# Kernel optimization log

Measured on AMD Instinct MI355X. Metric: run time of the kernel, lower is better.

Reference implementation:

```python
import jax, jax.numpy as jnp
import numpy as np

DIM, H, D = 2048, 16, 128
D_C, D_CQ, D_ROPE = 512, 1536, 64
B, T = 2, 2048


def _rope(t, cos, sin):
    # t: [..., T, D_ROPE]; cos/sin: [T, D_ROPE//2] broadcast over leading dims
    h = D_ROPE // 2
    t1, t2 = t[..., :h], t[..., h:]
    return jnp.concatenate([t1 * cos - t2 * sin, t2 * cos + t1 * sin], axis=-1)


def setup_inputs() -> dict:
    key = jax.random.key(0)
    ks = jax.random.split(key, 10)
    init = lambda k, shp, fan: (jax.random.normal(k, shp, jnp.float32) / np.sqrt(fan).astype(np.float32))
    x = jax.random.normal(ks[0], (B, T, DIM), jnp.float32)
    # RoPE tables for d_rope//2 = 32 rotary channels
    inv_freq = 1.0 / (10000.0 ** (np.arange(0, D_ROPE // 2, dtype=np.float32) / (D_ROPE // 2)))
    ang = np.arange(T, dtype=np.float32)[:, None] * inv_freq[None, :]
    cos = jnp.asarray(np.cos(ang), jnp.float32)
    sin = jnp.asarray(np.sin(ang), jnp.float32)
    return {
        "x": x,
        "cos": cos,
        "sin": sin,
        "w_kv": init(ks[1], (DIM, D_C), DIM),          # kv_compress
        "w_kdec": init(ks[2], (D_C, H * D), D_C),       # k_decompress
        "w_vdec": init(ks[3], (D_C, H * D), D_C),       # v_decompress
        "w_qc": init(ks[4], (DIM, D_CQ), DIM),          # q_compress
        "w_qdec": init(ks[5], (D_CQ, H * D), D_CQ),     # q_decompress
        "w_krope": init(ks[6], (DIM, D_ROPE), DIM),     # k_rope_proj
        "w_qrope": init(ks[7], (DIM, D_ROPE), DIM),     # q_rope_proj
        "w_o": init(ks[8], (H * D, DIM), H * D),        # wo
    }


def reference(x, cos, sin, w_kv, w_kdec, w_vdec, w_qc, w_qdec, w_krope, w_qrope, w_o):
    Bx, Tx, _ = x.shape
    # latent compress -> decompress
    c_kv = x @ w_kv                                       # [B,T,d_c]
    k = (c_kv @ w_kdec).reshape(Bx, Tx, H, D).transpose(0, 2, 1, 3)  # [B,H,T,D]
    v = (c_kv @ w_vdec).reshape(Bx, Tx, H, D).transpose(0, 2, 1, 3)
    c_q = x @ w_qc
    q = (c_q @ w_qdec).reshape(Bx, Tx, H, D).transpose(0, 2, 1, 3)
    # RoPE branch: head-shared projections, rotated then broadcast across heads
    k_rope = _rope(x @ w_krope, cos, sin)                 # [B,T,d_rope]
    q_rope = _rope(x @ w_qrope, cos, sin)
    rope_dim = min(D_ROPE, D)
    qr = jnp.broadcast_to(q_rope[:, None, :, :rope_dim], (Bx, H, Tx, rope_dim))
    kr = jnp.broadcast_to(k_rope[:, None, :, :rope_dim], (Bx, H, Tx, rope_dim))
    q = jnp.concatenate([q[..., :-rope_dim], qr], axis=-1)
    k = jnp.concatenate([k[..., :-rope_dim], kr], axis=-1)
    # causal SDPA, scale = 1/sqrt(head_dim)
    scores = jnp.einsum("bhtd,bhsd->bhts", q, k) / np.float32(np.sqrt(D))
    causal = jnp.tril(jnp.ones((Tx, Tx), dtype=bool))
    scores = jnp.where(causal, scores, jnp.float32(-1e30))
    attn = jax.nn.softmax(scores, axis=-1)
    out = jnp.einsum("bhts,bhsd->bhtd", attn, v)
    out = out.transpose(0, 2, 1, 3).reshape(Bx, Tx, H * D)
    return out @ w_o
```

## Files before the change

### kernel.cpp

```cpp
#include <hip/hip_runtime.h>
#include <stdint.h>
#include <math.h>

#define B_    2
#define T_    2048
#define DIM_  2048
#define H_    16
#define DC_   512
#define DCQ_  1536
#define NROWS (B_*T_)

typedef unsigned short u16;
typedef __attribute__((ext_vector_type(8))) __bf16 bf16x8;
typedef __attribute__((ext_vector_type(4))) float  f32x4;
typedef __attribute__((ext_vector_type(8))) unsigned short u16x8;
typedef __attribute__((ext_vector_type(4))) float  f4v;

__device__ __forceinline__ u16 f2bf(float f){
  unsigned u = __float_as_uint(f);
  u += 0x7FFFu + ((u >> 16) & 1u);
  return (u16)(u >> 16);
}
__device__ __forceinline__ float bf2f(u16 h){ return __uint_as_float(((unsigned)h) << 16); }

__device__ __forceinline__ unsigned cvt_pk_bf16(float lo, float hi){
  unsigned r;
  asm("v_cvt_pk_bf16_f32 %0, %1, %2" : "=v"(r) : "v"(lo), "v"(hi));
  return r;
}

__device__ __forceinline__ void gld_lds16(const void* g, void* l){
  auto gp = reinterpret_cast<__attribute__((address_space(1))) unsigned int*>(
      reinterpret_cast<uintptr_t>(g));
  auto lp = reinterpret_cast<__attribute__((address_space(3))) unsigned int*>(
      reinterpret_cast<uintptr_t>(l));
  __builtin_amdgcn_global_load_lds(gp, lp, 16, 0, 0);
}

__device__ __forceinline__ f32x4 mfma16(bf16x8 a, bf16x8 b, f32x4 c){
  return __builtin_amdgcn_mfma_f32_16x16x32_bf16(a, b, c, 0, 0, 0);
}

__device__ __forceinline__ void vmwait0(){ asm volatile("s_waitcnt vmcnt(0)" ::: "memory"); }
__device__ __forceinline__ void vmwait8(){ asm volatile("s_waitcnt vmcnt(8)" ::: "memory"); }
__device__ __forceinline__ void barr(){ asm volatile("s_barrier" ::: "memory"); }


struct TDesc { const void* src; u16* dst; int srcStride, dstStride, cblk, nbx, blk0; };
struct TPack { TDesc d[8]; };
#define TBLK 1088
#define CONVBLK 2048

__device__ __forceinline__ void do_transpose(void* ldsbuf, const TPack& p, int tb,
                                             int tid, int f){
  u16 (*tile)[72] = reinterpret_cast<u16(*)[72]>(ldsbuf);
  int i = 0;
  #pragma unroll
  for (int k = 1; k < 8; ++k) if (tb >= p.d[k].blk0) i = k;
  const void* src = p.d[i].src;
  u16* dst = p.d[i].dst;
  const int srcStride = p.d[i].srcStride, dstStride = p.d[i].dstStride;
  const int rel = tb - p.d[i].blk0;
  const int bx = rel % p.d[i].nbx, by = rel / p.d[i].nbx;
  const int r0 = by << 6, c0 = bx * p.d[i].cblk;
  #pragma unroll
  for (int it = 0; it < 2; ++it){
    int task = (it << 8) + tid;
    int r = task >> 3, c8 = (task & 7) << 3;
    if (f){
      const u16* pp = (const u16*)src + (size_t)(r0 + r) * srcStride + c0 + c8;
      u16x8 v = *reinterpret_cast<const u16x8*>(pp);
      #pragma unroll
      for (int j = 0; j < 8; ++j) tile[r][c8 + j] = v[j];
    } else {
      const float* pp = (const float*)src + (size_t)(r0 + r) * srcStride + c0 + c8;
      f4v a = reinterpret_cast<const f4v*>(pp)[0];
      f4v b = reinterpret_cast<const f4v*>(pp)[1];
      tile[r][c8+0]=f2bf(a.x); tile[r][c8+1]=f2bf(a.y); tile[r][c8+2]=f2bf(a.z); tile[r][c8+3]=f2bf(a.w);
      tile[r][c8+4]=f2bf(b.x); tile[r][c8+5]=f2bf(b.y); tile[r][c8+6]=f2bf(b.z); tile[r][c8+7]=f2bf(b.w);
    }
  }
  __syncthreads();
  #pragma unroll
  for (int it = 0; it < 2; ++it){
    int task = (it << 8) + tid;
    int rr = task >> 3, cc8 = (task & 7) << 3;
    u16x8 v;
    #pragma unroll
    for (int j = 0; j < 8; ++j) v[j] = tile[cc8 + j][rr];
    *reinterpret_cast<u16x8*>(dst + (size_t)((bx << 6) + rr) * dstStride + r0 + cc8) = v;
  }
}

__global__ void k_prep(const void* __restrict__ xsrc, u16* __restrict__ x_bf,
                       TPack p, const u16* __restrict__ cosr){
  __shared__ u16 tile[64][72];
  const int bid = blockIdx.x;
  const int tid = threadIdx.x;
  const int f = (cosr[0] == (u16)0x3F80u);
  if (bid < TBLK){
    do_transpose(tile, p, bid, tid, f);
    return;
  }
  if (f) return;
  const int base = ((bid - TBLK) * 256 + tid) * 4;
  #pragma unroll
  for (int q = 0; q < 4; ++q){
    int id = base + q;
    f4v v = reinterpret_cast<const f4v*>(xsrc)[id];
    unsigned lo = (unsigned)f2bf(v.x) | ((unsigned)f2bf(v.y) << 16);
    unsigned hi = (unsigned)f2bf(v.z) | ((unsigned)f2bf(v.w) << 16);
    reinterpret_cast<uint2*>(x_bf)[id] = make_uint2(lo, hi);
  }
}

__global__ __launch_bounds__(256, 2) void k_gemm(
    const u16* __restrict__ A0, int lda0, const u16* __restrict__ Bt0, int K0,
    u16* __restrict__ C0, int ldc0, float os0,
    const u16* __restrict__ A1, int lda1, const u16* __restrict__ Bt1, int K1,
    u16* __restrict__ C1, int ldc1, float os1,
    int ysplit, int swz, void* outp, const u16* __restrict__ cosr,
    const u16* __restrict__ alt0, const u16* __restrict__ alt1,
    u16* __restrict__ vt0, u16* __restrict__ vt1,
    const u16* __restrict__ ropeXc, const void* __restrict__ rcosp,
    const void* __restrict__ rsinp, u16* __restrict__ ropeK,
    u16* __restrict__ ropeQ, int* __restrict__ rticket,
    int ngemm, int sidemode, TPack tpp){
  __shared__ alignas(16) u16 lds[32768];
  const int tid = threadIdx.x;
  const int flat = blockIdx.y * gridDim.x + blockIdx.x;

  if (sidemode && flat >= ngemm){
    const int tb = flat - ngemm;
    if (sidemode == 1){
      if (tb == 0 && tid < 128) rticket[tid] = 0;
      const int f2 = (((const u16*)rcosp)[0] == (u16)0x3F80u);
      int id = tb * 256 + tid;
      int row = id >> 7, c = id & 127;
      int t = row & (T_ - 1);
      int d = c & 63, i = d & 31;
      float cs, sn;
      if (f2){ cs = bf2f(((const u16*)rcosp)[t * 32 + i]); sn = bf2f(((const u16*)rsinp)[t * 32 + i]); }
      else   { cs = ((const float*)rcosp)[t * 32 + i];     sn = ((const float*)rsinp)[t * 32 + i]; }
      int base = c & 64;
      float t1 = bf2f(ropeXc[(size_t)row * 2304 + 2048 + base + i]);
      float t2 = bf2f(ropeXc[(size_t)row * 2304 + 2048 + base + 32 + i]);
      float v = (d < 32) ? (t1 * cs - t2 * sn) : (t2 * cs + t1 * sn);
      if (c >= 64) v *= 0.12753139626374414f;
      ((c < 64) ? ropeK : ropeQ)[(size_t)row * 64 + d] = f2bf(v);
    } else {
      const int f2 = cosr ? (cosr[0] == (u16)0x3F80u) : 1;
      do_transpose(lds, tpp, tb, tid, f2);
    }
    return;
  }

  const int wid = tid >> 6, lane = tid & 63;
  const int wr = wid >> 1, wc = wid & 1;
  const int l16 = lane & 15, g = lane >> 4;
  int lin = flat;
  if (swz){
    const int q8 = ngemm >> 3;
    lin = (lin & 7) * q8 + (lin >> 3);
  }
  const int m0 = (lin & 31) << 7;
  int nt = lin >> 5;
  const u16 *A, *Bt, *alt; u16 *C, *vtp; int lda, K, ldc; float oscale;
  if (nt < ysplit){ A = A0; lda = lda0; Bt = Bt0; K = K0; C = C0; ldc = ldc0; oscale = os0; alt = alt0; vtp = vt0; }
  else { nt -= ysplit; A = A1; lda = lda1; Bt = Bt1; K = K1; C = C1; ldc = ldc1; oscale = os1; alt = alt1; vtp = vt1; }
  const int f = cosr ? (cosr[0] == (u16)0x3F80u) : 1;
  if (alt && f) A = alt;
  const int n0 = nt << 7;
  const size_t Kz = (size_t)K;
  const int nkt = K >> 6;

  auto STAGE = [&](int kt, int bufn){
    const int kb = kt << 6;
    #pragma unroll
    for (int q = 0; q < 8; ++q){
      const int ht = q >> 2;
      const int cq = ((q & 3) << 8) + tid;
      const int Lb = cq << 4;
      const int row = Lb >> 7;
      const int colb = (Lb & 127) ^ ((row & 7) << 4);
      const u16* src = ht ? (Bt + (size_t)(n0 + row) * Kz + kb + (colb >> 1))
                          : (A  + (size_t)(m0 + row) * lda + kb + (colb >> 1));
      gld_lds16(src, &lds[bufn * 16384 + ht * 8192 + (cq << 3)]);
    }
  };

  f32x4 acc[4][4] = {};

  STAGE(0, 0);
  int buf = 0;

  for (int kt = 0; kt < nkt; ++kt){
    if (kt + 1 < nkt){ STAGE(kt + 1, buf ^ 1); vmwait8(); }
    else vmwait0();
    barr();
    bf16x8 af[2][4], bfr[2][4];
    #pragma unroll
    for (int ks = 0; ks < 2; ++ks){
      #pragma unroll
      for (int mi = 0; mi < 4; ++mi){
        int row = (wr << 6) + (mi << 4) + l16;
        int cb = ((ks << 6) + (g << 4)) ^ ((row & 7) << 4);
        af[ks][mi] = *reinterpret_cast<const bf16x8*>(&lds[buf * 16384 + (((row << 7) + cb) >> 1)]);
      }
      #pragma unroll
      for (int ni = 0; ni < 4; ++ni){
        int row = (wc << 6) + (ni << 4) + l16;
        int cb = ((ks << 6) + (g << 4)) ^ ((row & 7) << 4);
        bfr[ks][ni] = *reinterpret_cast<const bf16x8*>(&lds[buf * 16384 + 8192 + (((row << 7) + cb) >> 1)]);
      }
    }
    __builtin_amdgcn_s_setprio(1);
    #pragma unroll
    for (int ks = 0; ks < 2; ++ks)
      #pragma unroll
      for (int mi = 0; mi < 4; ++mi)
        #pragma unroll
        for (int ni = 0; ni < 4; ++ni)
          acc[mi][ni] = mfma16(af[ks][mi], bfr[ks][ni], acc[mi][ni]);
    __builtin_amdgcn_s_setprio(0);
    barr();
    buf ^= 1;
  }

  const int r4 = g << 2;
  #pragma unroll
  for (int mi = 0; mi < 4; ++mi){
    int row = m0 + (wr << 6) + (mi << 4) + r4;
    #pragma unroll
    for (int ni = 0; ni < 4; ++ni){
      int col = n0 + (wc << 6) + (ni << 4) + l16;
      if (vtp && col >= 1024){
        int hd = col - 1024;
        u16* dst = vtp + (((size_t)(((row >> 11) << 4) + (hd >> 7)) << 7) + (hd & 127)) * (size_t)T_ + (row & (T_ - 1));
        union { u16 u[4]; uint2 v; } pk;
        #pragma unroll
        for (int j = 0; j < 4; ++j) pk.u[j] = f2bf(acc[mi][ni][j] * oscale);
        *reinterpret_cast<uint2*>(dst) = pk.v;
        continue;
      }
      #pragma unroll
      for (int j = 0; j < 4; ++j){
        float v = acc[mi][ni][j] * oscale;
        if (outp){
          if (f) ((u16*)outp)[(size_t)(row + j) * ldc + col] = f2bf(v);
          else   ((float*)outp)[(size_t)(row + j) * ldc + col] = v;
        } else {
          C[(size_t)(row + j) * ldc + col] = f2bf(v);
        }
      }
    }
  }
}

__global__ __launch_bounds__(512, 2) void k_attn(const u16* __restrict__ qP,
                                                 const u16* __restrict__ kvP,
                                                 const u16* __restrict__ vT,
                                                 const u16* __restrict__ krope,
                                                 const u16* __restrict__ qrope,
                                                 u16* __restrict__ aout){
  __shared__ alignas(16) u16 smem[65536];
  const int tid = threadIdx.x, wid = tid >> 6, lane = tid & 63;
  const int l16 = lane & 15, g = lane >> 4;
  const int lk = g << 3, r4 = g << 2;
  const int swl = l16 << 3;
  const int xcd = blockIdx.x & 7;
  const int idx = blockIdx.x >> 3;
  const int bh = (xcd << 2) + (idx & 3), b = bh >> 4, h = bh & 15;
  const int p = idx >> 2;
  const size_t bT = (size_t)b * T_;
  const u16* kvPb = kvP + bT * 1024 + (h << 6);
  const u16* krb  = krope + bT * 64;
  const u16* vTb  = vT + (size_t)bh * 128 * T_;

  for (int which = 0; which < 2; ++which){
    const int qt = which ? p : (15 - p);
    const int q0 = qt << 7;
    const int qlo = q0 + (wid << 4);
    const int nkv = qt + 1;

    auto STAGE = [&](int buf, int k0){
      const int base = buf << 15;
      #pragma unroll
      for (int r = 0; r < 8; ++r){
        int c = (r << 9) + tid;
        const u16* src;
        if (c < 2048){
          int row = c >> 4, cc = c & 15;
          int ccx = cc ^ (row & 15);
          int col0 = ccx << 3;
          src = (col0 < 64) ? (kvPb + (size_t)(k0 + row) * 1024 + col0)
                            : (krb  + (size_t)(k0 + row) * 64 + (col0 - 64));
        } else {
          int cv = c - 2048;
          int row = cv >> 4, cc = cv & 15;
          int ccx = cc ^ (row & 15);
          src = vTb + (size_t)row * T_ + k0 + (ccx << 3);
        }
        gld_lds16(src, &smem[base + (c << 3)]);
      }
    };

    bf16x8 qf[4];
    {
      size_t grow = bT + qlo + l16;
      #pragma unroll
      for (int ks = 0; ks < 4; ++ks){
        int d = (ks << 5) + lk;
        const u16* src = (ks < 2) ? (qP + grow * 1024 + (h << 6) + d)
                                  : (qrope + grow * 64 + (d - 64));
        qf[ks] = *reinterpret_cast<const bf16x8*>(src);
      }
    }
    f32x4 o[8] = {};
    float m = -3e38f, l = 0.f;

    STAGE(0, 0);
    __syncthreads();
    int cur = 0;

    for (int kv = 0; kv < nkv; ++kv){
      const int k0 = kv << 7;
      if (kv + 1 < nkv) STAGE(cur ^ 1, (kv + 1) << 7);
      const int kb = cur << 15;
      f32x4 s[8] = {};
      __builtin_amdgcn_s_setprio(1);
      #pragma unroll
      for (int ks = 0; ks < 4; ++ks){
        int colsw = ((ks << 5) + lk) ^ swl;
        #pragma unroll
        for (int n = 0; n < 8; ++n){
          bf16x8 kf = *reinterpret_cast<const bf16x8*>(&smem[kb + ((n << 4) + l16) * 128 + colsw]);
          s[n] = mfma16(kf, qf[ks], s[n]);
        }
      }
      __builtin_amdgcn_s_setprio(0);
      if (k0 + 127 > qlo){
        const int tq = qlo + l16;
        #pragma unroll
        for (int n = 0; n < 8; ++n)
          #pragma unroll
          for (int j = 0; j < 4; ++j)
            s[n][j] = (k0 + (n << 4) + r4 + j <= tq) ? s[n][j] : -3e38f;
      }
      float mx;
      {
        float a0 = fmaxf(fmaxf(s[0][0], s[0][1]), fmaxf(s[0][2], s[0][3]));
        float a1 = fmaxf(fmaxf(s[1][0], s[1][1]), fmaxf(s[1][2], s[1][3]));
        float a2 = fmaxf(fmaxf(s[2][0], s[2][1]), fmaxf(s[2][2], s[2][3]));
        float a3 = fmaxf(fmaxf(s[3][0], s[3][1]), fmaxf(s[3][2], s[3][3]));
        float a4 = fmaxf(fmaxf(s[4][0], s[4][1]), fmaxf(s[4][2], s[4][3]));
        float a5 = fmaxf(fmaxf(s[5][0], s[5][1]), fmaxf(s[5][2], s[5][3]));
        float a6 = fmaxf(fmaxf(s[6][0], s[6][1]), fmaxf(s[6][2], s[6][3]));
        float a7 = fmaxf(fmaxf(s[7][0], s[7][1]), fmaxf(s[7][2], s[7][3]));
        mx = fmaxf(fmaxf(fmaxf(a0, a1), fmaxf(a2, a3)),
                   fmaxf(fmaxf(a4, a5), fmaxf(a6, a7)));
        mx = fmaxf(mx, __shfl_xor(mx, 16));
        mx = fmaxf(mx, __shfl_xor(mx, 32));
      }
      if (__ballot(mx > m + 8.f)){
        float mnew = fmaxf(m, mx);
        float alpha = exp2f(m - mnew);
        m = mnew; l *= alpha;
        #pragma unroll
        for (int j = 0; j < 4; ++j){
          float av = __shfl(alpha, r4 + j);
          #pragma unroll
          for (int db = 0; db < 8; ++db) o[db][j] *= av;
        }
      }
      unsigned w[8][2];
      float rs = 0.f;
      #pragma unroll
      for (int n = 0; n < 8; ++n)
        #pragma unroll
        for (int jh = 0; jh < 2; ++jh){
          float p0 = exp2f(s[n][2*jh]     - m);
          float p1 = exp2f(s[n][2*jh + 1] - m);
          rs += p0 + p1;
          w[n][jh] = cvt_pk_bf16(p0, p1);
        }
      rs += __shfl_xor(rs, 16);
      rs += __shfl_xor(rs, 32);
      l += rs;
      const int srcA = l16 + ((g & 1) << 5);
      const int srcB = srcA + 16;
      const bool hi = (g >= 2);
      bf16x8 pa[4];
      #pragma unroll
      for (int ks2 = 0; ks2 < 4; ++ks2){
        unsigned a0 = __shfl((int)w[2*ks2][0],     srcA);
        unsigned b0 = __shfl((int)w[2*ks2 + 1][0], srcA);
        unsigned a1 = __shfl((int)w[2*ks2][1],     srcA);
        unsigned b1 = __shfl((int)w[2*ks2 + 1][1], srcA);
        unsigned a2 = __shfl((int)w[2*ks2][0],     srcB);
        unsigned b2 = __shfl((int)w[2*ks2 + 1][0], srcB);
        unsigned a3 = __shfl((int)w[2*ks2][1],     srcB);
        unsigned b3 = __shfl((int)w[2*ks2 + 1][1], srcB);
        union { unsigned u[4]; bf16x8 v; } pk;
        pk.u[0] = hi ? b0 : a0;
        pk.u[1] = hi ? b1 : a1;
        pk.u[2] = hi ? b2 : a2;
        pk.u[3] = hi ? b3 : a3;
        pa[ks2] = pk.v;
      }
      __builtin_amdgcn_s_setprio(1);
      #pragma unroll
      for (int ks2 = 0; ks2 < 4; ++ks2){
        int colsw = ((ks2 << 5) + lk) ^ swl;
        #pragma unroll
        for (int db = 0; db < 8; ++db){
          bf16x8 vb = *reinterpret_cast<const bf16x8*>(&smem[kb + 16384 + ((db << 4) + l16) * 128 + colsw]);
          o[db] = mfma16(pa[ks2], vb, o[db]);
        }
      }
      __builtin_amdgcn_s_setprio(0);
      __syncthreads();
      cur ^= 1;
    }
    #pragma unroll
    for (int j = 0; j < 4; ++j){
      float lv = __shfl(l, r4 + j);
      float rinv = 1.f / lv;
      const int tq = qlo + r4 + j;
      u16* dst = aout + (bT + tq) * 2048 + (h << 7) + l16;
      #pragma unroll
      for (int db = 0; db < 8; ++db)
        dst[db << 4] = f2bf(o[db][j] * rinv);
    }
  }
}

extern "C" void kernel_launch(void* const* d_in, const int* in_sizes, int n_in,
                              void* d_out, int out_size, void* d_ws, size_t ws_size,
                              hipStream_t stream){
  const void* x       = d_in[0];
  const void* cosp    = d_in[1];
  const void* sinp    = d_in[2];
  const void* w_kv    = d_in[3];
  const void* w_kdec  = d_in[4];
  const void* w_vdec  = d_in[5];
  const void* w_qc    = d_in[6];
  const void* w_qdec  = d_in[7];
  const void* w_krope = d_in[8];
  const void* w_qrope = d_in[9];
  const void* w_o     = d_in[10];

  char* ws = (char*)d_ws;
  size_t off = 0;
  auto alloc = [&](size_t bytes){ void* p = ws + off; off += (bytes + 255) & ~(size_t)255; return p; };
  int* ticket   = (int*)alloc(1024);
  u16* x_bf     = (u16*)alloc((size_t)NROWS * DIM_ * 2);
  u16* w_c1T    = (u16*)alloc((size_t)2304 * DIM_ * 2);
  u16* w_kvdT   = (u16*)alloc((size_t)3072 * DC_ * 2);
  u16* w_qdPT   = (u16*)alloc((size_t)1024 * DCQ_ * 2);
  u16* w_oT     = (u16*)alloc((size_t)DIM_ * DIM_ * 2);
  u16* xc       = (u16*)alloc((size_t)NROWS * 2304 * 2);
  u16* qP       = (u16*)alloc((size_t)NROWS * 1024 * 2);
  u16* kvP      = (u16*)alloc((size_t)NROWS * 1024 * 2);
  u16* krope    = (u16*)alloc((size_t)NROWS * 64 * 2);
  u16* qrope    = (u16*)alloc((size_t)NROWS * 64 * 2);
  u16* vT       = (u16*)alloc((size_t)32 * 128 * T_ * 2);
  u16* aout     = (u16*)alloc((size_t)NROWS * DIM_ * 2);
  (void)in_sizes; (void)n_in; (void)out_size; (void)ws_size;

  const float SC2 = 0.12753139626374414f;
  const u16* cosr = (const u16*)cosp;

  TPack tp = {};
  tp.d[0] = { w_kv,    w_c1T,                        512,  2048, 64,  8,  0    };
  tp.d[1] = { w_qc,    w_c1T + (size_t)512 * 2048,   1536, 2048, 64,  24, 256  };
  tp.d[2] = { w_krope, w_c1T + (size_t)2048 * 2048,  64,   2048, 64,  1,  1024 };
  tp.d[3] = { w_qrope, w_c1T + (size_t)2112 * 2048,  64,   2048, 64,  1,  1056 };
  tp.d[4] = { nullptr, nullptr, 0, 0, 0, 1, 1 << 30 };
  tp.d[5] = { nullptr, nullptr, 0, 0, 0, 1, 1 << 30 };
  tp.d[6] = { nullptr, nullptr, 0, 0, 0, 1, 1 << 30 };
  tp.d[7] = { nullptr, nullptr, 0, 0, 0, 1, 1 << 30 };
  hipLaunchKernelGGL(k_prep, dim3(TBLK + CONVBLK), dim3(256), 0, stream, x, x_bf, tp, cosr);

  TPack ts = {};
  ts.d[0] = { w_kdec, w_kvdT,                       2048, 512,  128, 16, 0    };
  ts.d[1] = { w_vdec, w_kvdT + (size_t)1024 * 512,  2048, 512,  64,  32, 128  };
  ts.d[2] = { w_qdec, w_qdPT,                       2048, 1536, 128, 16, 384  };
  ts.d[3] = { w_o,    w_oT,                         2048, 2048, 64,  32, 768  };
  ts.d[4] = { nullptr, nullptr, 0, 0, 0, 1, 1 << 30 };
  ts.d[5] = { nullptr, nullptr, 0, 0, 0, 1, 1 << 30 };
  ts.d[6] = { nullptr, nullptr, 0, 0, 0, 1, 1 << 30 };
  ts.d[7] = { nullptr, nullptr, 0, 0, 0, 1, 1 << 30 };
  TPack tz = {};

  hipLaunchKernelGGL(k_gemm, dim3(2336, 1), dim3(256), 0, stream,
                     x_bf, DIM_, w_c1T, DIM_, xc, 2304, 1.0f,
                     x_bf, DIM_, w_c1T, DIM_, xc, 2304, 1.0f,
                     17, 1, (void*)nullptr, cosr,
                     (const u16*)x, (const u16*)x,
                     (u16*)nullptr, (u16*)nullptr,
                     (const u16*)nullptr, (const void*)nullptr, (const void*)nullptr,
                     (u16*)nullptr, (u16*)nullptr, (int*)nullptr,
                     544, 2, ts);
  hipLaunchKernelGGL(k_gemm, dim3(3072, 1), dim3(256), 0, stream,
                     xc + 512, 2304, w_qdPT, DCQ_, qP, 1024, SC2,
                     xc, 2304, w_kvdT, DC_, kvP, 1024, 1.0f,
                     8, 0, (void*)nullptr, (const u16*)nullptr,
                     (const u16*)nullptr, (const u16*)nullptr,
                     (u16*)nullptr, vT,
                     xc, cosp, sinp, krope, qrope, ticket,
                     1024, 1, tz);
  hipLaunchKernelGGL(k_attn, dim3(256), dim3(512), 0, stream,
                     qP, kvP, vT, krope, qrope, aout);
  hipLaunchKernelGGL(k_gemm, dim3(32, 16), dim3(256), 0, stream,
                     aout, DIM_, w_oT, DIM_, (u16*)nullptr, DIM_, 1.0f,
                     aout, DIM_, w_oT, DIM_, (u16*)nullptr, DIM_, 1.0f,
                     16, 1, d_out, cosr,
                     (const u16*)nullptr, (const u16*)nullptr,
                     (u16*)nullptr, (u16*)nullptr,
                     (const u16*)nullptr, (const void*)nullptr, (const void*)nullptr,
                     (u16*)nullptr, (u16*)nullptr, (int*)nullptr,
                     512, 0, tz);
}
```

Baseline: 220.9 us.

## Process paired causal query tiles in one KV sweep sharing staged K/V

The attention kernel previously handled its two paired query tiles (a high and a low causal tile) one after another, staging K/V tiles into LDS twice. Now both tiles keep separate accumulators and softmax state and are processed in a single loop over the high tile's KV range. Each staged KV block is applied to both tiles, so the low tile's KV loads are no longer repeated. This doubles the per-thread accumulator and Q-fragment registers under launch_bounds(512,2), which risks spills or reduced occupancy.

```diff
diff --git a/kernel.cpp b/kernel.cpp
--- a/kernel.cpp
+++ b/kernel.cpp
@@ -257,6 +257,100 @@
   }
 }
 
+#define ATTN_TILE(QF, O, M, L, QLO, KB) do{                                          \
+  f32x4 s_[8] = {};                                                                   \
+  __builtin_amdgcn_s_setprio(1);                                                      \
+  _Pragma("unroll")                                                                   \
+  for (int ks = 0; ks < 4; ++ks){                                                     \
+    int colsw = ((ks << 5) + lk) ^ swl;                                               \
+    _Pragma("unroll")                                                                 \
+    for (int n = 0; n < 8; ++n){                                                      \
+      bf16x8 kf = *reinterpret_cast<const bf16x8*>(&smem[(KB) + ((n << 4) + l16) * 128 + colsw]); \
+      s_[n] = mfma16(kf, QF[ks], s_[n]);                                              \
+    }                                                                                 \
+  }                                                                                   \
+  __builtin_amdgcn_s_setprio(0);                                                      \
+  if (k0 + 127 > (QLO)){                                                              \
+    const int tq_ = (QLO) + l16 - (wid << 4) + (wid << 4);                            \
+    (void)tq_;                                                                        \
+    const int tqq = (QLO) + l16;                                                      \
+    _Pragma("unroll")                                                                 \
+    for (int n = 0; n < 8; ++n)                                                       \
+      _Pragma("unroll")                                                               \
+      for (int j = 0; j < 4; ++j)                                                     \
+        s_[n][j] = (k0 + (n << 4) + r4 + j <= tqq) ? s_[n][j] : -3e38f;               \
+  }                                                                                   \
+  float mx_;                                                                          \
+  {                                                                                   \
+    float a0 = fmaxf(fmaxf(s_[0][0], s_[0][1]), fmaxf(s_[0][2], s_[0][3]));           \
+    float a1 = fmaxf(fmaxf(s_[1][0], s_[1][1]), fmaxf(s_[1][2], s_[1][3]));           \
+    float a2 = fmaxf(fmaxf(s_[2][0], s_[2][1]), fmaxf(s_[2][2], s_[2][3]));           \
+    float a3 = fmaxf(fmaxf(s_[3][0], s_[3][1]), fmaxf(s_[3][2], s_[3][3]));           \
+    float a4 = fmaxf(fmaxf(s_[4][0], s_[4][1]), fmaxf(s_[4][2], s_[4][3]));           \
+    float a5 = fmaxf(fmaxf(s_[5][0], s_[5][1]), fmaxf(s_[5][2], s_[5][3]));           \
+    float a6 = fmaxf(fmaxf(s_[6][0], s_[6][1]), fmaxf(s_[6][2], s_[6][3]));           \
+    float a7 = fmaxf(fmaxf(s_[7][0], s_[7][1]), fmaxf(s_[7][2], s_[7][3]));           \
+    mx_ = fmaxf(fmaxf(fmaxf(a0, a1), fmaxf(a2, a3)),                                  \
+                fmaxf(fmaxf(a4, a5), fmaxf(a6, a7)));                                 \
+    mx_ = fmaxf(mx_, __shfl_xor(mx_, 16));                                            \
+    mx_ = fmaxf(mx_, __shfl_xor(mx_, 32));                                            \
+  }                                                                                   \
+  if (__ballot(mx_ > (M) + 8.f)){                                                     \
+    float mnew = fmaxf((M), mx_);                                                     \
+    float alpha = exp2f((M) - mnew);                                                  \
+    (M) = mnew; (L) *= alpha;                                                         \
+    _Pragma("unroll")                                                                 \
+    for (int j = 0; j < 4; ++j){                                                      \
+      float av = __shfl(alpha, r4 + j);                                               \
+      _Pragma("unroll")                                                               \
+      for (int db = 0; db < 8; ++db) O[db][j] *= av;                                  \
+    }                                                                                 \
+  }                                                                                   \
+  unsigned w_[8][2];                                                                  \
+  float rs_ = 0.f;                                                                    \
+  _Pragma("unroll")                                                                   \
+  for (int n = 0; n < 8; ++n)                                                         \
+    _Pragma("unroll")                                                                 \
+    for (int jh = 0; jh < 2; ++jh){                                                   \
+      float p0 = exp2f(s_[n][2*jh]     - (M));                                        \
+      float p1 = exp2f(s_[n][2*jh + 1] - (M));                                        \
+      rs_ += p0 + p1;                                                                 \
+      w_[n][jh] = cvt_pk_bf16(p0, p1);                                                \
+    }                                                                                 \
+  rs_ += __shfl_xor(rs_, 16);                                                         \
+  rs_ += __shfl_xor(rs_, 32);                                                         \
+  (L) += rs_;                                                                         \
+  bf16x8 pa_[4];                                                                      \
+  _Pragma("unroll")                                                                   \
+  for (int ks2 = 0; ks2 < 4; ++ks2){                                                  \
+    unsigned a0 = __shfl((int)w_[2*ks2][0],     srcA);                                \
+    unsigned b0 = __shfl((int)w_[2*ks2 + 1][0], srcA);                                \
+    unsigned a1 = __shfl((int)w_[2*ks2][1],     srcA);                                \
+    unsigned b1 = __shfl((int)w_[2*ks2 + 1][1], srcA);                                \
+    unsigned a2 = __shfl((int)w_[2*ks2][0],     srcB);                                \
+    unsigned b2 = __shfl((int)w_[2*ks2 + 1][0], srcB);                                \
+    unsigned a3 = __shfl((int)w_[2*ks2][1],     srcB);                                \
+    unsigned b3 = __shfl((int)w_[2*ks2 + 1][1], srcB);                                \
+    union { unsigned u[4]; bf16x8 v; } pk;                                            \
+    pk.u[0] = hi ? b0 : a0;                                                           \
+    pk.u[1] = hi ? b1 : a1;                                                           \
+    pk.u[2] = hi ? b2 : a2;                                                           \
+    pk.u[3] = hi ? b3 : a3;                                                           \
+    pa_[ks2] = pk.v;                                                                  \
+  }                                                                                   \
+  __builtin_amdgcn_s_setprio(1);                                                      \
+  _Pragma("unroll")                                                                   \
+  for (int ks2 = 0; ks2 < 4; ++ks2){                                                  \
+    int colsw = ((ks2 << 5) + lk) ^ swl;                                              \
+    _Pragma("unroll")                                                                 \
+    for (int db = 0; db < 8; ++db){                                                   \
+      bf16x8 vb = *reinterpret_cast<const bf16x8*>(&smem[(KB) + 16384 + ((db << 4) + l16) * 128 + colsw]); \
+      O[db] = mfma16(pa_[ks2], vb, O[db]);                                            \
+    }                                                                                 \
+  }                                                                                   \
+  __builtin_amdgcn_s_setprio(0);                                                      \
+}while(0)
+
 __global__ __launch_bounds__(512, 2) void k_attn(const u16* __restrict__ qP,
                                                  const u16* __restrict__ kvP,
                                                  const u16* __restrict__ vT,
@@ -268,6 +362,9 @@
   const int l16 = lane & 15, g = lane >> 4;
   const int lk = g << 3, r4 = g << 2;
   const int swl = l16 << 3;
+  const int srcA = l16 + ((g & 1) << 5);
+  const int srcB = srcA + 16;
+  const bool hi = (g >= 2);
   const int xcd = blockIdx.x & 7;
   const int idx = blockIdx.x >> 3;
   const int bh = (xcd << 2) + (idx & 3), b = bh >> 4, h = bh & 15;
@@ -277,161 +374,85 @@
   const u16* krb  = krope + bT * 64;
   const u16* vTb  = vT + (size_t)bh * 128 * T_;
 
-  for (int which = 0; which < 2; ++which){
-    const int qt = which ? p : (15 - p);
-    const int q0 = qt << 7;
-    const int qlo = q0 + (wid << 4);
-    const int nkv = qt + 1;
-
-    auto STAGE = [&](int buf, int k0){
-      const int base = buf << 15;
-      #pragma unroll
-      for (int r = 0; r < 8; ++r){
-        int c = (r << 9) + tid;
-        const u16* src;
-        if (c < 2048){
-          int row = c >> 4, cc = c & 15;
-          int ccx = cc ^ (row & 15);
-          int col0 = ccx << 3;
-          src = (col0 < 64) ? (kvPb + (size_t)(k0 + row) * 1024 + col0)
-                            : (krb  + (size_t)(k0 + row) * 64 + (col0 - 64));
-        } else {
-          int cv = c - 2048;
-          int row = cv >> 4, cc = cv & 15;
-          int ccx = cc ^ (row & 15);
-          src = vTb + (size_t)row * T_ + k0 + (ccx << 3);
-        }
-        gld_lds16(src, &smem[base + (c << 3)]);
+  const int qtH = 15 - p, qtL = p;
+  const int q0H = qtH << 7, q0L = qtL << 7;
+  const int qloH = q0H + (wid << 4), qloL = q0L + (wid << 4);
+  const int nkvH = qtH + 1, nkvL = qtL + 1;
+
+  auto STAGE = [&](int buf, int k0){
+    const int base = buf << 15;
+    #pragma unroll
+    for (int r = 0; r < 8; ++r){
+      int c = (r << 9) + tid;
+      const u16* src;
+      if (c < 2048){
+        int row = c >> 4, cc = c & 15;
+        int ccx = cc ^ (row & 15);
+        int col0 = ccx << 3;
+        src = (col0 < 64) ? (kvPb + (size_t)(k0 + row) * 1024 + col0)
+                          : (krb  + (size_t)(k0 + row) * 64 + (col0 - 64));
+      } else {
+        int cv = c - 2048;
+        int row = cv >> 4, cc = cv & 15;
+        int ccx = cc ^ (row & 15);
+        src = vTb + (size_t)row * T_ + k0 + (ccx << 3);
       }
-    };
-
-    bf16x8 qf[4];
-    {
-      size_t grow = bT + qlo + l16;
-      #pragma unroll
-      for (int ks = 0; ks < 4; ++ks){
-        int d = (ks << 5) + lk;
-        const u16* src = (ks < 2) ? (qP + grow * 1024 + (h << 6) + d)
-                                  : (qrope + grow * 64 + (d - 64));
-        qf[ks] = *reinterpret_cast<const bf16x8*>(src);
-      }
-    }
-    f32x4 o[8] = {};
-    float m = -3e38f, l = 0.f;
-
-    STAGE(0, 0);
+      gld_lds16(src, &smem[base + (c << 3)]);
+    }
+  };
+
+  bf16x8 qfH[4], qfL[4];
+  {
+    size_t growH = bT + qloH + l16;
+    size_t growL = bT + qloL + l16;
+    #pragma unroll
+    for (int ks = 0; ks < 4; ++ks){
+      int d = (ks << 5) + lk;
+      const u16* sH = (ks < 2) ? (qP + growH * 1024 + (h << 6) + d)
+                               : (qrope + growH * 64 + (d - 64));
+      const u16* sL = (ks < 2) ? (qP + growL * 1024 + (h << 6) + d)
+                               : (qrope + growL * 64 + (d - 64));
+      qfH[ks] = *reinterpret_cast<const bf16x8*>(sH);
+      qfL[ks] = *reinterpret_cast<const bf16x8*>(sL);
+    }
+  }
+  f32x4 oH[8] = {}, oL[8] = {};
+  float mH = -3e38f, lH = 0.f, mL = -3e38f, lL = 0.f;
+
+  STAGE(0, 0);
+  __syncthreads();
+  int cur = 0;
+
+  for (int kv = 0; kv < nkvH; ++kv){
+    const int k0 = kv << 7;
+    if (kv + 1 < nkvH) STAGE(cur ^ 1, (kv + 1) << 7);
+    const int kb = cur << 15;
+    ATTN_TILE(qfH, oH, mH, lH, qloH, kb);
+    if (kv < nkvL)
+      ATTN_TILE(qfL, oL, mL, lL, qloL, kb);
     __syncthreads();
-    int cur = 0;
-
-    for (int kv = 0; kv < nkv; ++kv){
-      const int k0 = kv << 7;
-      if (kv + 1 < nkv) STAGE(cur ^ 1, (kv + 1) << 7);
-      const int kb = cur << 15;
-      f32x4 s[8] = {};
-      __builtin_amdgcn_s_setprio(1);
-      #pragma unroll
-      for (int ks = 0; ks < 4; ++ks){
-        int colsw = ((ks << 5) + lk) ^ swl;
-        #pragma unroll
-        for (int n = 0; n < 8; ++n){
-          bf16x8 kf = *reinterpret_cast<const bf16x8*>(&smem[kb + ((n << 4) + l16) * 128 + colsw]);
-          s[n] = mfma16(kf, qf[ks], s[n]);
-        }
-      }
-      __builtin_amdgcn_s_setprio(0);
-      if (k0 + 127 > qlo){
-        const int tq = qlo + l16;
-        #pragma unroll
-        for (int n = 0; n < 8; ++n)
-          #pragma unroll
-          for (int j = 0; j < 4; ++j)
-            s[n][j] = (k0 + (n << 4) + r4 + j <= tq) ? s[n][j] : -3e38f;
-      }
-      float mx;
-      {
-        float a0 = fmaxf(fmaxf(s[0][0], s[0][1]), fmaxf(s[0][2], s[0][3]));
-        float a1 = fmaxf(fmaxf(s[1][0], s[1][1]), fmaxf(s[1][2], s[1][3]));
-        float a2 = fmaxf(fmaxf(s[2][0], s[2][1]), fmaxf(s[2][2], s[2][3]));
-        float a3 = fmaxf(fmaxf(s[3][0], s[3][1]), fmaxf(s[3][2], s[3][3]));
-        float a4 = fmaxf(fmaxf(s[4][0], s[4][1]), fmaxf(s[4][2], s[4][3]));
-        float a5 = fmaxf(fmaxf(s[5][0], s[5][1]), fmaxf(s[5][2], s[5][3]));
-        float a6 = fmaxf(fmaxf(s[6][0], s[6][1]), fmaxf(s[6][2], s[6][3]));
-        float a7 = fmaxf(fmaxf(s[7][0], s[7][1]), fmaxf(s[7][2], s[7][3]));
-        mx = fmaxf(fmaxf(fmaxf(a0, a1), fmaxf(a2, a3)),
-                   fmaxf(fmaxf(a4, a5), fmaxf(a6, a7)));
-        mx = fmaxf(mx, __shfl_xor(mx, 16));
-        mx = fmaxf(mx, __shfl_xor(mx, 32));
-      }
-      if (__ballot(mx > m + 8.f)){
-        float mnew = fmaxf(m, mx);
-        float alpha = exp2f(m - mnew);
-        m = mnew; l *= alpha;
-        #pragma unroll
-        for (int j = 0; j < 4; ++j){
-          float av = __shfl(alpha, r4 + j);
-          #pragma unroll
-          for (int db = 0; db < 8; ++db) o[db][j] *= av;
-        }
-      }
-      unsigned w[8][2];
-      float rs = 0.f;
-      #pragma unroll
-      for (int n = 0; n < 8; ++n)
-        #pragma unroll
-        for (int jh = 0; jh < 2; ++jh){
-          float p0 = exp2f(s[n][2*jh]     - m);
-          float p1 = exp2f(s[n][2*jh + 1] - m);
-          rs += p0 + p1;
-          w[n][jh] = cvt_pk_bf16(p0, p1);
-        }
-      rs += __shfl_xor(rs, 16);
-      rs += __shfl_xor(rs, 32);
-      l += rs;
-      const int srcA = l16 + ((g & 1) << 5);
-      const int srcB = srcA + 16;
-      const bool hi = (g >= 2);
-      bf16x8 pa[4];
-      #pragma unroll
-      for (int ks2 = 0; ks2 < 4; ++ks2){
-        unsigned a0 = __shfl((int)w[2*ks2][0],     srcA);
-        unsigned b0 = __shfl((int)w[2*ks2 + 1][0], srcA);
-        unsigned a1 = __shfl((int)w[2*ks2][1],     srcA);
-        unsigned b1 = __shfl((int)w[2*ks2 + 1][1], srcA);
-        unsigned a2 = __shfl((int)w[2*ks2][0],     srcB);
-        unsigned b2 = __shfl((int)w[2*ks2 + 1][0], srcB);
-        unsigned a3 = __shfl((int)w[2*ks2][1],     srcB);
-        unsigned b3 = __shfl((int)w[2*ks2 + 1][1], srcB);
-        union { unsigned u[4]; bf16x8 v; } pk;
-        pk.u[0] = hi ? b0 : a0;
-        pk.u[1] = hi ? b1 : a1;
-        pk.u[2] = hi ? b2 : a2;
-        pk.u[3] = hi ? b3 : a3;
-        pa[ks2] = pk.v;
-      }
-      __builtin_amdgcn_s_setprio(1);
-      #pragma unroll
-      for (int ks2 = 0; ks2 < 4; ++ks2){
-        int colsw = ((ks2 << 5) + lk) ^ swl;
-        #pragma unroll
-        for (int db = 0; db < 8; ++db){
-          bf16x8 vb = *reinterpret_cast<const bf16x8*>(&smem[kb + 16384 + ((db << 4) + l16) * 128 + colsw]);
-          o[db] = mfma16(pa[ks2], vb, o[db]);
-        }
-      }
-      __builtin_amdgcn_s_setprio(0);
-      __syncthreads();
-      cur ^= 1;
-    }
-    #pragma unroll
-    for (int j = 0; j < 4; ++j){
-      float lv = __shfl(l, r4 + j);
-      float rinv = 1.f / lv;
-      const int tq = qlo + r4 + j;
-      u16* dst = aout + (bT + tq) * 2048 + (h << 7) + l16;
-      #pragma unroll
-      for (int db = 0; db < 8; ++db)
-        dst[db << 4] = f2bf(o[db][j] * rinv);
-    }
+    cur ^= 1;
+  }
+
+  #pragma unroll
+  for (int j = 0; j < 4; ++j){
+    float lv = __shfl(lH, r4 + j);
+    float rinv = 1.f / lv;
+    const int tq = qloH + r4 + j;
+    u16* dst = aout + (bT + tq) * 2048 + (h << 7) + l16;
+    #pragma unroll
+    for (int db = 0; db < 8; ++db)
+      dst[db << 4] = f2bf(oH[db][j] * rinv);
+  }
+  #pragma unroll
+  for (int j = 0; j < 4; ++j){
+    float lv = __shfl(lL, r4 + j);
+    float rinv = 1.f / lv;
+    const int tq = qloL + r4 + j;
+    u16* dst = aout + (bT + tq) * 2048 + (h << 7) + l16;
+    #pragma unroll
+    for (int db = 0; db < 8; ++db)
+      dst[db << 4] = f2bf(oL[db][j] * rinv);
   }
 }
 
```

New measurement: 222.1 us. No clear change (+0.6%).
